# Kernel optimization log

Hardware: AMD Instinct MI355X
Metric: run time of the kernel (lower is better)

## Reference

```python
import jax, jax.numpy as jnp
import numpy as np

N = 10000      # atoms
E = 320000     # edges (avg degree 32)
C = 128        # hidden_channels
NB = 32        # num_basis
L = 3          # num_layers
CUT = 5.0      # cutoff
G = 8          # graphs in batch


def setup_inputs() -> dict:
    key = jax.random.key(0)
    ks = jax.random.split(key, 32)
    pos = jax.random.normal(ks[0], (N, 3), dtype=jnp.float32) * 2.0
    z = jax.random.randint(ks[1], (N,), 0, 100)
    row = jax.random.randint(ks[2], (E,), 0, N)
    # avoid self-loops so edge_length > 0
    col = (row + 1 + jax.random.randint(ks[3], (E,), 0, N - 1)) % N
    edge_index = jnp.stack([row, col])
    shifts = jnp.zeros((E, 3), dtype=jnp.float32)
    batch_index = jnp.sort(jax.random.randint(ks[4], (N,), 0, G))
    s = 0.05
    p = lambda k, shape: jax.random.normal(k, shape, dtype=jnp.float32) * s
    return {
        'z': z, 'pos': pos, 'edge_index': edge_index, 'shifts': shifts,
        'batch_index': batch_index,
        'emb': p(ks[5], (100, C)),
        # message blocks (stacked over layers)
        'm_w1': p(ks[6], (L, C, C)), 'm_b1': p(ks[7], (L, C)),
        'm_w2': p(ks[8], (L, C, 3 * C)), 'm_b2': p(ks[9], (L, 3 * C)),
        'f_w': p(ks[10], (L, NB, 3 * C)), 'f_b': p(ks[11], (L, 3 * C)),
        # update blocks
        'u_w': p(ks[12], (L, C, C)), 'v_w': p(ks[13], (L, C, C)),
        'up_w1': p(ks[14], (L, 2 * C, C)), 'up_b1': p(ks[15], (L, C)),
        'up_w2': p(ks[16], (L, C, 3 * C)), 'up_b2': p(ks[17], (L, 3 * C)),
        # readout
        'r_w1': p(ks[18], (C, C // 2)), 'r_b1': p(ks[19], (C // 2,)),
        'r_w2': p(ks[20], (C // 2, 1)), 'r_b2': p(ks[21], (1,)),
    }


def painn_energy(pos, shifts, emb, m_w1, m_b1, m_w2, m_b2, f_w, f_b,
                 u_w, v_w, up_w1, up_b1, up_w2, up_b2,
                 r_w1, r_b1, r_w2, r_b2, z, edge_index, batch_index):
    row, col = edge_index[0], edge_index[1]
    scalar = emb[z]                                  # [N, C]
    vector = jnp.zeros((N, 3, C), dtype=pos.dtype)   # [N, 3, C]

    edge_vec = pos[col] - pos[row] + shifts          # [E, 3]
    edge_len = jnp.sqrt(jnp.sum(edge_vec * edge_vec, axis=-1) + 1e-12)  # [E]
    direction = edge_vec / edge_len[:, None]

    # smooth bump envelope (C-inf, compact support)
    scaled = edge_len / CUT
    inside = scaled < 1.0
    denom = jnp.where(inside, 1.0 - scaled * scaled, 1.0)
    gate = jnp.where(inside, jnp.exp(1.0 - 1.0 / denom), 0.0)  # [E]

    # gaussian radial basis
    centers = jnp.linspace(0.0, CUT, NB)
    gamma = 1.0 / (centers[1] - centers[0]) ** 2
    rbf = jnp.exp(-gamma * (edge_len[:, None] - centers) ** 2)  # [E, NB]
    edge_attr = rbf * gate[:, None]

    for l in range(L):
        # --- message ---
        h = jax.nn.silu(scalar[col] @ m_w1[l] + m_b1[l]) @ m_w2[l] + m_b2[l]  # [E, 3C]
        w = h * (edge_attr @ f_w[l] + f_b[l]) * gate[:, None]
        w1, w2, w3 = jnp.split(w, 3, axis=-1)                                 # each [E, C]
        d_scalar = jax.ops.segment_sum(w1, row, num_segments=N)
        msg_vec = vector[col] * w2[:, None, :] + w3[:, None, :] * direction[:, :, None]  # [E,3,C]
        d_vector = jax.ops.segment_sum(msg_vec, row, num_segments=N)
        scalar = scalar + d_scalar
        vector = vector + d_vector
        # --- update ---
        uv = vector @ u_w[l]                                   # [N, 3, C]
        vv = vector @ v_w[l]
        v_norm = jnp.sqrt(jnp.sum(vv * vv, axis=1) + 1e-8)     # [N, C]
        a = jax.nn.silu(jnp.concatenate([scalar, v_norm], axis=-1) @ up_w1[l] + up_b1[l]) @ up_w2[l] + up_b2[l]
        a1, a2, a3 = jnp.split(a, 3, axis=-1)
        scalar = scalar + a1 + a2 * jnp.sum(uv * vv, axis=1)
        vector = vector + a3[:, None, :] * uv

    e_atom = jax.nn.silu(scalar @ r_w1 + r_b1) @ r_w2 + r_b2   # [N, 1]
    return jax.ops.segment_sum(e_atom, batch_index, num_segments=G)  # [G, 1]


def reference(z, pos, edge_index, shifts, batch_index, emb,
              m_w1, m_b1, m_w2, m_b2, f_w, f_b,
              u_w, v_w, up_w1, up_b1, up_w2, up_b2,
              r_w1, r_b1, r_w2, r_b2):
    return painn_energy(pos, shifts, emb, m_w1, m_b1, m_w2, m_b2, f_w, f_b,
                        u_w, v_w, up_w1, up_b1, up_w2, up_b2,
                        r_w1, r_b1, r_w2, r_b2, z, edge_index, batch_index)
```

## Files before the change

kernel.cpp:

```cpp
#include <hip/hip_runtime.h>
#include <math.h>

#define CUTR 5.0f
#define TL 2048
#define NBASIS 32
#define HSC 16.0f
#define TSC 16.0f
#define VSC 64.0f
#define INV_HT (1.0f / (HSC * TSC))
#define INV_HTV (1.0f / (HSC * TSC * VSC))

typedef __attribute__((ext_vector_type(8))) short bf16x8;
typedef __attribute__((ext_vector_type(4))) float f32x4;
typedef __attribute__((ext_vector_type(2))) float f32x2;

struct U3 { uint x, y, z; };

__device__ __forceinline__ float silu_f(float x) { return x / (1.0f + expf(-x)); }
__device__ __forceinline__ ushort f2bf(float x) {
  uint b = __float_as_uint(x);
  uint r = (b + 0x7FFFu + ((b >> 16) & 1u)) >> 16;
  return (ushort)r;
}
__device__ __forceinline__ float bf2f(ushort u) { return __uint_as_float((uint)u << 16); }
__device__ __forceinline__ uchar f2fp8(float x) {
  return (uchar)(__builtin_amdgcn_cvt_pk_fp8_f32(x, 0.0f, 0, false) & 0xff);
}
__device__ __forceinline__ f32x2 fp8lo(uint u) {
  return __builtin_amdgcn_cvt_pk_f32_fp8((int)u, false);
}
__device__ __forceinline__ f32x2 fp8hi(uint u) {
  return __builtin_amdgcn_cvt_pk_f32_fp8((int)u, true);
}

__global__ __launch_bounds__(384) void table_kernel(const float* __restrict__ f_w,
                                                    const float* __restrict__ f_b,
                                                    uchar* __restrict__ tab) {
  __shared__ float fws[NBASIS * 384];
  __shared__ float rbf[8][NBASIS];
  __shared__ float gv[8];
  int tid = threadIdx.x;
  int bi = blockIdx.x;
  int l = bi >> 8, tb = bi & 255;
  for (int i = tid; i < NBASIS * 384; i += 384) fws[i] = f_w[l * NBASIS * 384 + i];
  if (tid < 256) {
    int tt = tid >> 5, k = tid & 31;
    float len = (float)(tb * 8 + tt) * (CUTR / (float)(TL - 1));
    const float gamma = (31.0f / 5.0f) * (31.0f / 5.0f);
    float c = 5.0f * (float)k / 31.0f;
    float d = len - c;
    rbf[tt][k] = expf(-gamma * d * d);
    if (k == 0) {
      float s = len * (1.0f / CUTR);
      gv[tt] = (s < 1.0f) ? expf(1.0f - 1.0f / (1.0f - s * s)) : 0.0f;
    }
  }
  __syncthreads();
  int j = tid % 384;
  int b = j >> 7, ch = j & 127;
  float fb = f_b[l * 384 + j];
  for (int tt = 0; tt < 8; ++tt) {
    float acc = 0.0f;
#pragma unroll
    for (int k = 0; k < NBASIS; ++k) acc += rbf[tt][k] * fws[k * 384 + j];
    float g = gv[tt];
    tab[((size_t)l * TL + (size_t)(tb * 8 + tt)) * 512 + (ch >> 1) * 8 + b * 2 + (ch & 1)] =
        f2fp8(g * (g * acc + fb) * TSC);
  }
}

__global__ __launch_bounds__(256) void init_kernel(
    const int* __restrict__ z, const float* __restrict__ emb, float* __restrict__ scalar,
    ushort* __restrict__ sbf, const float* __restrict__ m_w1, const float* __restrict__ m_w2,
    const float* __restrict__ u_w, const float* __restrict__ v_w,
    const float* __restrict__ up_w1, const float* __restrict__ up_w2,
    const float* __restrict__ r_w1, ushort* __restrict__ wt, const float* __restrict__ pos,
    const int* __restrict__ ei, const float* __restrict__ shifts, int* __restrict__ counts,
    int N, int E) {
  int tid = threadIdx.x;
  int bi = blockIdx.x;
  int nbEmb = (N * 128 + 255) / 256;
  int nbW = (548864 + 255) / 256;
  if (bi < nbEmb) {
    int idx = bi * 256 + tid;
    if (idx >= N * 128) return;
    int n = idx >> 7, j = idx & 127;
    float v = emb[z[n] * 128 + j];
    scalar[idx] = v;
    sbf[idx] = f2bf(v);
    return;
  }
  bi -= nbEmb;
  if (bi < nbW) {
    int idx = bi * 256 + tid;
    if (idx >= 548864) return;
    float v;
    if (idx >= 540672) {
      int t = idx - 540672;
      int n = t >> 7, k = t & 127;
      v = r_w1[k * 64 + n];
    } else {
      int l = idx / 180224, local = idx % 180224;
      if (local < 16384) {
        int n = local >> 7, k = local & 127;
        v = m_w1[l * 16384 + k * 128 + n];
      } else if (local < 65536) {
        int t = local - 16384;
        int n = t >> 7, k = t & 127;
        v = m_w2[l * 49152 + k * 384 + n];
      } else if (local < 98304) {
        int t = local - 65536;
        int n = t >> 7, k = t & 127;
        v = (n < 128) ? u_w[l * 16384 + k * 128 + n] : v_w[l * 16384 + k * 128 + (n - 128)];
      } else if (local < 131072) {
        int t = local - 98304;
        int n = t >> 8, k = t & 255;
        v = up_w1[l * 32768 + k * 128 + n];
      } else {
        int t = local - 131072;
        int n = t >> 7, k = t & 127;
        v = up_w2[l * 49152 + k * 384 + n];
      }
    }
    wt[idx] = f2bf(v);
    return;
  }
  bi -= nbW;
  {
    int e = bi * 256 + tid;
    if (e >= E) return;
    int r = ei[e], c = ei[E + e];
    float dx = pos[c * 3 + 0] - pos[r * 3 + 0] + shifts[e * 3 + 0];
    float dy = pos[c * 3 + 1] - pos[r * 3 + 1] + shifts[e * 3 + 1];
    float dz = pos[c * 3 + 2] - pos[r * 3 + 2] + shifts[e * 3 + 2];
    float len = sqrtf(dx * dx + dy * dy + dz * dz + 1e-12f);
    if (len < CUTR) atomicAdd(&counts[r], 1);
  }
}

__global__ __launch_bounds__(1024) void scan_kernel(const int* __restrict__ counts,
                                                    int* __restrict__ offs,
                                                    int* __restrict__ cursor, int N) {
  __shared__ int sm[1024];
  int tid = threadIdx.x;
  int CH = (N + 1023) / 1024;
  int base = tid * CH;
  int sum = 0;
  for (int i = 0; i < CH; i++) sum += (base + i < N) ? counts[base + i] : 0;
  sm[tid] = sum;
  __syncthreads();
  for (int o = 1; o < 1024; o <<= 1) {
    int v = (tid >= o) ? sm[tid - o] : 0;
    __syncthreads();
    sm[tid] += v;
    __syncthreads();
  }
  int run = sm[tid] - sum;
  for (int i = 0; i < CH; i++) {
    if (base + i < N) {
      offs[base + i] = run;
      cursor[base + i] = run;
      run += counts[base + i];
    }
  }
  if (tid == 1023) offs[N] = sm[1023];
}

__global__ void fill_kernel(const float* __restrict__ pos, const int* __restrict__ ei,
                            const float* __restrict__ shifts, int* __restrict__ cursor,
                            float4* __restrict__ pk, int E) {
  int e = blockIdx.x * 256 + threadIdx.x;
  if (e >= E) return;
  int r = ei[e], c = ei[E + e];
  float dx = pos[c * 3 + 0] - pos[r * 3 + 0] + shifts[e * 3 + 0];
  float dy = pos[c * 3 + 1] - pos[r * 3 + 1] + shifts[e * 3 + 1];
  float dz = pos[c * 3 + 2] - pos[r * 3 + 2] + shifts[e * 3 + 2];
  float len = sqrtf(dx * dx + dy * dy + dz * dz + 1e-12f);
  if (len >= CUTR) return;
  float inv = 1.0f / len;
  float x = len * ((float)(TL - 1) / CUTR);
  int ib = (int)(x + 0.5f);
  if (ib > TL - 1) ib = TL - 1;
  int p = atomicAdd(&cursor[r], 1);
  pk[p] = make_float4(__int_as_float(c | (ib << 14)), dx * inv, dy * inv, dz * inv);
}

__global__ __launch_bounds__(256) void message_kernel(
    const int* __restrict__ offs, const float4* __restrict__ pk, const uchar* __restrict__ hv8,
    const uchar* __restrict__ tab8, float* __restrict__ scalar, ushort* __restrict__ sbf,
    float* __restrict__ vec, ushort* __restrict__ vbout, int N) {
  int lane = threadIdx.x & 63;
  int n = blockIdx.x * 4 + (threadIdx.x >> 6);
  if (n >= N) return;
  int p0 = offs[n], p1 = offs[n + 1];
  float aS0 = 0.f, aS1 = 0.f;
  float aW00 = 0.f, aW01 = 0.f, aW10 = 0.f, aW11 = 0.f, aW20 = 0.f, aW21 = 0.f;
  float aD00 = 0.f, aD01 = 0.f, aD10 = 0.f, aD11 = 0.f, aD20 = 0.f, aD21 = 0.f;
  int p = p0;
  bool hasA = p < p1, hasB = p + 1 < p1;
  float4 cA, cB;
  if (hasA) cA = pk[p];
  if (hasB) cB = pk[p + 1];
  while (hasA) {
    int bitsA = __float_as_int(cA.x);
    int colA = bitsA & 16383, ibA = bitsA >> 14;
    U3 hvA = *(const U3*)(hv8 + (size_t)colA * 768 + lane * 12);
    uint2 tA = *(const uint2*)(tab8 + (size_t)ibA * 512 + lane * 8);
    U3 hvB;
    uint2 tB;
    float4 dB;
    if (hasB) {
      int bitsB = __float_as_int(cB.x);
      int colB = bitsB & 16383, ibB = bitsB >> 14;
      dB = cB;
      hvB = *(const U3*)(hv8 + (size_t)colB * 768 + lane * 12);
      tB = *(const uint2*)(tab8 + (size_t)ibB * 512 + lane * 8);
    }
    int pn = p + 2;
    bool nA = pn < p1, nB = pn + 1 < p1;
    float4 fA, fB;
    if (nA) fA = pk[pn];
    if (nB) fB = pk[pn + 1];
    {
      f32x2 h1 = fp8lo(hvA.x), h2 = fp8hi(hvA.x);
      f32x2 h3 = fp8lo(hvA.y), v0 = fp8hi(hvA.y);
      f32x2 v1 = fp8lo(hvA.z), v2 = fp8hi(hvA.z);
      f32x2 t1 = fp8lo(tA.x), t2 = fp8hi(tA.x), t3 = fp8lo(tA.y);
      aS0 += h1.x * t1.x;
      aS1 += h1.y * t1.y;
      float w2l = h2.x * t2.x, w2h = h2.y * t2.y;
      float w3l = h3.x * t3.x, w3h = h3.y * t3.y;
      aW00 += v0.x * w2l; aW01 += v0.y * w2h;
      aW10 += v1.x * w2l; aW11 += v1.y * w2h;
      aW20 += v2.x * w2l; aW21 += v2.y * w2h;
      aD00 += w3l * cA.y; aD01 += w3h * cA.y;
      aD10 += w3l * cA.z; aD11 += w3h * cA.z;
      aD20 += w3l * cA.w; aD21 += w3h * cA.w;
    }
    if (hasB) {
      f32x2 h1 = fp8lo(hvB.x), h2 = fp8hi(hvB.x);
      f32x2 h3 = fp8lo(hvB.y), v0 = fp8hi(hvB.y);
      f32x2 v1 = fp8lo(hvB.z), v2 = fp8hi(hvB.z);
      f32x2 t1 = fp8lo(tB.x), t2 = fp8hi(tB.x), t3 = fp8lo(tB.y);
      aS0 += h1.x * t1.x;
      aS1 += h1.y * t1.y;
      float w2l = h2.x * t2.x, w2h = h2.y * t2.y;
      float w3l = h3.x * t3.x, w3h = h3.y * t3.y;
      aW00 += v0.x * w2l; aW01 += v0.y * w2h;
      aW10 += v1.x * w2l; aW11 += v1.y * w2h;
      aW20 += v2.x * w2l; aW21 += v2.y * w2h;
      aD00 += w3l * dB.y; aD01 += w3h * dB.y;
      aD10 += w3l * dB.z; aD11 += w3h * dB.z;
      aD20 += w3l * dB.w; aD21 += w3h * dB.w;
    }
    cA = fA;
    cB = fB;
    hasA = nA;
    hasB = nB;
    p = pn;
  }
  float sS0 = aS0 * INV_HT, sS1 = aS1 * INV_HT;
  float sV00 = aW00 * INV_HTV + aD00 * INV_HT;
  float sV01 = aW01 * INV_HTV + aD01 * INV_HT;
  float sV10 = aW10 * INV_HTV + aD10 * INV_HT;
  float sV11 = aW11 * INV_HTV + aD11 * INV_HT;
  float sV20 = aW20 * INV_HTV + aD20 * INV_HT;
  float sV21 = aW21 * INV_HTV + aD21 * INV_HT;
  float2* sp = (float2*)(scalar + (size_t)n * 128) + lane;
  float2 sv = *sp;
  sv.x += sS0;
  sv.y += sS1;
  *sp = sv;
  ((uint*)(sbf + (size_t)n * 128))[lane] = (uint)f2bf(sv.x) | ((uint)f2bf(sv.y) << 16);
  float2* vp0 = (float2*)(vec + (size_t)n * 384) + lane;
  float2* vp1 = (float2*)(vec + (size_t)n * 384 + 128) + lane;
  float2* vp2 = (float2*)(vec + (size_t)n * 384 + 256) + lane;
  float2 v0 = *vp0, v1 = *vp1, v2 = *vp2;
  v0.x += sV00; v0.y += sV01;
  v1.x += sV10; v1.y += sV11;
  v2.x += sV20; v2.y += sV21;
  *vp0 = v0; *vp1 = v1; *vp2 = v2;
  uint* ob = (uint*)(vbout + (size_t)n * 384);
  ob[lane] = (uint)f2bf(v0.x) | ((uint)f2bf(v0.y) << 16);
  ob[lane + 64] = (uint)f2bf(v1.x) | ((uint)f2bf(v1.y) << 16);
  ob[lane + 128] = (uint)f2bf(v2.x) | ((uint)f2bf(v2.y) << 16);
}

__global__ __launch_bounds__(512) void mlp_kernel(const ushort* __restrict__ A,
                                                  const ushort* __restrict__ W1T,
                                                  const float* __restrict__ b1,
                                                  const ushort* __restrict__ W2T,
                                                  const float* __restrict__ b2,
                                                  uchar* __restrict__ out, int M) {
  __shared__ ushort As[32 * 128];
  __shared__ ushort Bs[128 * 128];
  __shared__ ushort Hs[32 * 128];
  int tid = threadIdx.x;
  int lane = tid & 63, w = tid >> 6;
  int mh = w >> 2, wc = w & 3;
  int m0 = blockIdx.x * 32;
  int cl = lane & 15, rq = lane >> 4;
  int ra = mh * 16 + cl;
  f32x4 acc[2] = {};
  {
    {
      int row = tid >> 4, ch = tid & 15;
      uint4 av = make_uint4(0, 0, 0, 0);
      if (m0 + row < M) av = *(const uint4*)(A + (size_t)(m0 + row) * 128 + ch * 8);
      *(uint4*)(&As[row * 128 + ((ch ^ (row & 7)) * 8)]) = av;
    }
#pragma unroll
    for (int r = 0; r < 4; ++r) {
      int c = tid + r * 512;
      int row = c >> 4, ch = c & 15;
      uint4 bv = *(const uint4*)(W1T + (size_t)row * 128 + ch * 8);
      *(uint4*)(&Bs[row * 128 + ((ch ^ (row & 7)) * 8)]) = bv;
    }
    __syncthreads();
#pragma unroll
    for (int ks = 0; ks < 4; ++ks) {
      int ch = ks * 4 + rq;
      bf16x8 a = *(bf16x8*)&As[ra * 128 + ((ch ^ (ra & 7)) * 8)];
#pragma unroll
      for (int ns = 0; ns < 2; ++ns) {
        int rb = wc * 32 + ns * 16 + cl;
        bf16x8 b = *(bf16x8*)&Bs[rb * 128 + ((ch ^ (rb & 7)) * 8)];
        acc[ns] = __builtin_amdgcn_mfma_f32_16x16x32_bf16(a, b, acc[ns], 0, 0, 0);
      }
    }
  }
#pragma unroll
  for (int ns = 0; ns < 2; ++ns) {
    int hcol = wc * 32 + ns * 16 + cl;
    float bv = b1[hcol];
    int chunk = hcol >> 3, el = hcol & 7;
#pragma unroll
    for (int j = 0; j < 4; ++j) {
      int hr = mh * 16 + rq * 4 + j;
      float v = silu_f(acc[ns][j] + bv);
      Hs[hr * 128 + ((chunk ^ (hr & 7)) * 8) + el] = f2bf(v);
    }
  }
  __syncthreads();
  for (int nt = 0; nt < 3; ++nt) {
#pragma unroll
    for (int r = 0; r < 4; ++r) {
      int c = tid + r * 512;
      int row = c >> 4, ch = c & 15;
      uint4 bv = *(const uint4*)(W2T + (size_t)(nt * 128 + row) * 128 + ch * 8);
      *(uint4*)(&Bs[row * 128 + ((ch ^ (row & 7)) * 8)]) = bv;
    }
    __syncthreads();
    f32x4 acc2[2] = {};
#pragma unroll
    for (int ks = 0; ks < 4; ++ks) {
      int ch = ks * 4 + rq;
      bf16x8 a = *(bf16x8*)&Hs[ra * 128 + ((ch ^ (ra & 7)) * 8)];
#pragma unroll
      for (int ns = 0; ns < 2; ++ns) {
        int rb = wc * 32 + ns * 16 + cl;
        bf16x8 b = *(bf16x8*)&Bs[rb * 128 + ((ch ^ (rb & 7)) * 8)];
        acc2[ns] = __builtin_amdgcn_mfma_f32_16x16x32_bf16(a, b, acc2[ns], 0, 0, 0);
      }
    }
#pragma unroll
    for (int ns = 0; ns < 2; ++ns) {
      int ch = wc * 32 + ns * 16 + cl;
      float bv = b2[nt * 128 + ch];
#pragma unroll
      for (int j = 0; j < 4; ++j) {
        int m = m0 + mh * 16 + rq * 4 + j;
        if (m >= M) continue;
        out[(size_t)m * 768 + (ch >> 1) * 12 + nt * 2 + (ch & 1)] =
            f2fp8((acc2[ns][j] + bv) * HSC);
      }
    }
    __syncthreads();
  }
}

__global__ __launch_bounds__(512) void mlp2_kernel(const ushort* __restrict__ sbf_in,
                                                   const ushort* __restrict__ W1T,
                                                   const float* __restrict__ b1,
                                                   const ushort* __restrict__ W2T,
                                                   const float* __restrict__ b2,
                                                   const ushort* __restrict__ uvvv,
                                                   float* __restrict__ scalar,
                                                   ushort* __restrict__ sbf,
                                                   float* __restrict__ vec,
                                                   uchar* __restrict__ vbf8, int M) {
  __shared__ ushort As[32 * 128];
  __shared__ ushort Bs[128 * 128];
  __shared__ ushort Hs[32 * 128];
  int tid = threadIdx.x;
  int lane = tid & 63, w = tid >> 6;
  int mh = w >> 2, wc = w & 3;
  int m0 = blockIdx.x * 32;
  int cl = lane & 15, rq = lane >> 4;
  int ra = mh * 16 + cl;
  f32x4 acc[2] = {};
  for (int k0 = 0; k0 < 256; k0 += 128) {
    __syncthreads();
    {
      int row = tid >> 4, ch = tid & 15;
      uint4 av = make_uint4(0, 0, 0, 0);
      if (m0 + row < M) {
        if (k0 == 0) {
          av = *(const uint4*)(sbf_in + (size_t)(m0 + row) * 128 + ch * 8);
        } else {
          const ushort* ub = uvvv + (size_t)(m0 + row) * 768 + 128 + ch * 8;
          bf16x8 x0 = *(const bf16x8*)(ub);
          bf16x8 x1 = *(const bf16x8*)(ub + 256);
          bf16x8 x2 = *(const bf16x8*)(ub + 512);
          ushort pkv[8];
#pragma unroll
          for (int e = 0; e < 8; ++e) {
            float a = bf2f((ushort)x0[e]), bb = bf2f((ushort)x1[e]), cc = bf2f((ushort)x2[e]);
            pkv[e] = f2bf(sqrtf(a * a + bb * bb + cc * cc + 1e-8f));
          }
          av = *(uint4*)pkv;
        }
      }
      *(uint4*)(&As[row * 128 + ((ch ^ (row & 7)) * 8)]) = av;
    }
#pragma unroll
    for (int r = 0; r < 4; ++r) {
      int c = tid + r * 512;
      int row = c >> 4, ch = c & 15;
      uint4 bv = *(const uint4*)(W1T + (size_t)row * 256 + k0 + ch * 8);
      *(uint4*)(&Bs[row * 128 + ((ch ^ (row & 7)) * 8)]) = bv;
    }
    __syncthreads();
#pragma unroll
    for (int ks = 0; ks < 4; ++ks) {
      int ch = ks * 4 + rq;
      bf16x8 a = *(bf16x8*)&As[ra * 128 + ((ch ^ (ra & 7)) * 8)];
#pragma unroll
      for (int ns = 0; ns < 2; ++ns) {
        int rb = wc * 32 + ns * 16 + cl;
        bf16x8 b = *(bf16x8*)&Bs[rb * 128 + ((ch ^ (rb & 7)) * 8)];
        acc[ns] = __builtin_amdgcn_mfma_f32_16x16x32_bf16(a, b, acc[ns], 0, 0, 0);
      }
    }
  }
#pragma unroll
  for (int ns = 0; ns < 2; ++ns) {
    int hcol = wc * 32 + ns * 16 + cl;
    float bv = b1[hcol];
    int chunk = hcol >> 3, el = hcol & 7;
#pragma unroll
    for (int j = 0; j < 4; ++j) {
      int hr = mh * 16 + rq * 4 + j;
      float v = silu_f(acc[ns][j] + bv);
      Hs[hr * 128 + ((chunk ^ (hr & 7)) * 8) + el] = f2bf(v);
    }
  }
  __syncthreads();
  f32x4 aReg[3][2];
  for (int nt = 0; nt < 3; ++nt) {
#pragma unroll
    for (int r = 0; r < 4; ++r) {
      int c = tid + r * 512;
      int row = c >> 4, ch = c & 15;
      uint4 bv = *(const uint4*)(W2T + (size_t)(nt * 128 + row) * 128 + ch * 8);
      *(uint4*)(&Bs[row * 128 + ((ch ^ (row & 7)) * 8)]) = bv;
    }
    __syncthreads();
    f32x4 acc2[2] = {};
#pragma unroll
    for (int ks = 0; ks < 4; ++ks) {
      int ch = ks * 4 + rq;
      bf16x8 a = *(bf16x8*)&Hs[ra * 128 + ((ch ^ (ra & 7)) * 8)];
#pragma unroll
      for (int ns = 0; ns < 2; ++ns) {
        int rb = wc * 32 + ns * 16 + cl;
        bf16x8 b = *(bf16x8*)&Bs[rb * 128 + ((ch ^ (rb & 7)) * 8)];
        acc2[ns] = __builtin_amdgcn_mfma_f32_16x16x32_bf16(a, b, acc2[ns], 0, 0, 0);
      }
    }
#pragma unroll
    for (int ns = 0; ns < 2; ++ns) aReg[nt][ns] = acc2[ns];
    __syncthreads();
  }
#pragma unroll
  for (int ns = 0; ns < 2; ++ns) {
    int chOff = wc * 32 + ns * 16 + cl;
    float b2a = b2[chOff], b2b = b2[128 + chOff], b2c = b2[256 + chOff];
#pragma unroll
    for (int j = 0; j < 4; ++j) {
      int nn = m0 + mh * 16 + rq * 4 + j;
      if (nn >= M) continue;
      float a1 = aReg[0][ns][j] + b2a;
      float a2 = aReg[1][ns][j] + b2b;
      float a3 = aReg[2][ns][j] + b2c;
      const ushort* ub = uvvv + (size_t)nn * 768;
      float uv0 = bf2f(ub[chOff]), vv0 = bf2f(ub[128 + chOff]);
      float uv1 = bf2f(ub[256 + chOff]), vv1 = bf2f(ub[384 + chOff]);
      float uv2 = bf2f(ub[512 + chOff]), vv2 = bf2f(ub[640 + chOff]);
      float dot = uv0 * vv0 + uv1 * vv1 + uv2 * vv2;
      size_t si = (size_t)nn * 128 + chOff;
      float s = scalar[si] + a1 + a2 * dot;
      scalar[si] = s;
      sbf[si] = f2bf(s);
      size_t vb = (size_t)nn * 384 + chOff;
      float nv0 = vec[vb] + a3 * uv0;
      float nv1 = vec[vb + 128] + a3 * uv1;
      float nv2 = vec[vb + 256] + a3 * uv2;
      vec[vb] = nv0;
      vec[vb + 128] = nv1;
      vec[vb + 256] = nv2;
      size_t hb = (size_t)nn * 768 + (chOff >> 1) * 12 + 6 + (chOff & 1);
      vbf8[hb] = f2fp8(nv0 * VSC);
      vbf8[hb + 2] = f2fp8(nv1 * VSC);
      vbf8[hb + 4] = f2fp8(nv2 * VSC);
    }
  }
}

__global__ __launch_bounds__(256) void gemm_kernel(const ushort* __restrict__ A,
                                                   const ushort* __restrict__ WT,
                                                   ushort* __restrict__ Cout, int M, int K,
                                                   int Nn) {
  __shared__ ushort As[64 * 128];
  __shared__ ushort Bs[64 * 128];
  int tid = threadIdx.x;
  int m0 = blockIdx.x * 64, n0 = blockIdx.y * 64;
  int lane = tid & 63, w = tid >> 6, wr = w >> 1, wc = w & 1;
  f32x4 acc[2][2] = {};
  for (int k0 = 0; k0 < K; k0 += 128) {
    __syncthreads();
#pragma unroll
    for (int r = 0; r < 4; ++r) {
      int c = tid + r * 256;
      int row = c >> 4, col16 = c & 15;
      uint4 av = make_uint4(0, 0, 0, 0);
      if (m0 + row < M) av = *(const uint4*)(A + (size_t)(m0 + row) * K + k0 + col16 * 8);
      *(uint4*)(&As[row * 128 + ((col16 ^ (row & 7)) * 8)]) = av;
      uint4 bv = *(const uint4*)(WT + (size_t)(n0 + row) * K + k0 + col16 * 8);
      *(uint4*)(&Bs[row * 128 + ((col16 ^ (row & 7)) * 8)]) = bv;
    }
    __syncthreads();
#pragma unroll
    for (int ks = 0; ks < 4; ++ks) {
      int ch = ks * 4 + (lane >> 4);
      int ra0 = wr * 32 + (lane & 15), ra1 = ra0 + 16;
      int rb0 = wc * 32 + (lane & 15), rb1 = rb0 + 16;
      bf16x8 a0 = *(bf16x8*)&As[ra0 * 128 + ((ch ^ (ra0 & 7)) * 8)];
      bf16x8 a1 = *(bf16x8*)&As[ra1 * 128 + ((ch ^ (ra1 & 7)) * 8)];
      bf16x8 b0 = *(bf16x8*)&Bs[rb0 * 128 + ((ch ^ (rb0 & 7)) * 8)];
      bf16x8 b1 = *(bf16x8*)&Bs[rb1 * 128 + ((ch ^ (rb1 & 7)) * 8)];
      acc[0][0] = __builtin_amdgcn_mfma_f32_16x16x32_bf16(a0, b0, acc[0][0], 0, 0, 0);
      acc[0][1] = __builtin_amdgcn_mfma_f32_16x16x32_bf16(a0, b1, acc[0][1], 0, 0, 0);
      acc[1][0] = __builtin_amdgcn_mfma_f32_16x16x32_bf16(a1, b0, acc[1][0], 0, 0, 0);
      acc[1][1] = __builtin_amdgcn_mfma_f32_16x16x32_bf16(a1, b1, acc[1][1], 0, 0, 0);
    }
  }
  int cl = lane & 15, rq = lane >> 4;
#pragma unroll
  for (int ms = 0; ms < 2; ++ms)
#pragma unroll
    for (int ns = 0; ns < 2; ++ns) {
      int n = n0 + wc * 32 + ns * 16 + cl;
#pragma unroll
      for (int j = 0; j < 4; ++j) {
        int m = m0 + wr * 32 + ms * 16 + rq * 4 + j;
        if (m >= M) continue;
        Cout[(size_t)m * Nn + n] = f2bf(acc[ms][ns][j]);
      }
    }
}

__global__ __launch_bounds__(256) void readout_kernel(
    const ushort* __restrict__ sbf, const ushort* __restrict__ r1T, const float* __restrict__ rb1,
    const float* __restrict__ r_w2, const float* __restrict__ r_b2, const int* __restrict__ bidx,
    float* __restrict__ out, int N, int G) {
  __shared__ ushort As[64 * 128];
  __shared__ ushort Bs[64 * 128];
  __shared__ float rs[64];
  __shared__ float sm[64];
  int tid = threadIdx.x;
  int m0 = blockIdx.x * 64;
  int lane = tid & 63, w = tid >> 6, wr = w >> 1, wc = w & 1;
  int cl = lane & 15, rq = lane >> 4;
#pragma unroll
  for (int r = 0; r < 4; ++r) {
    int c = tid + r * 256;
    int row = c >> 4, ch = c & 15;
    uint4 av = make_uint4(0, 0, 0, 0);
    if (m0 + row < N) av = *(const uint4*)(sbf + (size_t)(m0 + row) * 128 + ch * 8);
    *(uint4*)(&As[row * 128 + ((ch ^ (row & 7)) * 8)]) = av;
    uint4 bv = *(const uint4*)(r1T + (size_t)row * 128 + ch * 8);
    *(uint4*)(&Bs[row * 128 + ((ch ^ (row & 7)) * 8)]) = bv;
  }
  if (tid < 64) {
    rs[tid] = 0.f;
    sm[tid] = 0.f;
  }
  __syncthreads();
  f32x4 acc[2][2] = {};
#pragma unroll
  for (int ks = 0; ks < 4; ++ks) {
    int ch = ks * 4 + rq;
    int ra0 = wr * 32 + cl, ra1 = ra0 + 16;
    int rb0 = wc * 32 + cl, rb1 = rb0 + 16;
    bf16x8 a0 = *(bf16x8*)&As[ra0 * 128 + ((ch ^ (ra0 & 7)) * 8)];
    bf16x8 a1 = *(bf16x8*)&As[ra1 * 128 + ((ch ^ (ra1 & 7)) * 8)];
    bf16x8 b0 = *(bf16x8*)&Bs[rb0 * 128 + ((ch ^ (rb0 & 7)) * 8)];
    bf16x8 b1 = *(bf16x8*)&Bs[rb1 * 128 + ((ch ^ (rb1 & 7)) * 8)];
    acc[0][0] = __builtin_amdgcn_mfma_f32_16x16x32_bf16(a0, b0, acc[0][0], 0, 0, 0);
    acc[0][1] = __builtin_amdgcn_mfma_f32_16x16x32_bf16(a0, b1, acc[0][1], 0, 0, 0);
    acc[1][0] = __builtin_amdgcn_mfma_f32_16x16x32_bf16(a1, b0, acc[1][0], 0, 0, 0);
    acc[1][1] = __builtin_amdgcn_mfma_f32_16x16x32_bf16(a1, b1, acc[1][1], 0, 0, 0);
  }
#pragma unroll
  for (int ms = 0; ms < 2; ++ms) {
    float part0 = 0.f, part1 = 0.f, part2 = 0.f, part3 = 0.f;
#pragma unroll
    for (int ns = 0; ns < 2; ++ns) {
      int col = wc * 32 + ns * 16 + cl;
      float b1v = rb1[col], wv = r_w2[col];
      part0 += silu_f(acc[ms][ns][0] + b1v) * wv;
      part1 += silu_f(acc[ms][ns][1] + b1v) * wv;
      part2 += silu_f(acc[ms][ns][2] + b1v) * wv;
      part3 += silu_f(acc[ms][ns][3] + b1v) * wv;
    }
#pragma unroll
    for (int o = 1; o < 16; o <<= 1) {
      part0 += __shfl_xor(part0, o);
      part1 += __shfl_xor(part1, o);
      part2 += __shfl_xor(part2, o);
      part3 += __shfl_xor(part3, o);
    }
    if (cl == 0) {
      int rbase = wr * 32 + ms * 16 + rq * 4;
      atomicAdd(&rs[rbase + 0], part0);
      atomicAdd(&rs[rbase + 1], part1);
      atomicAdd(&rs[rbase + 2], part2);
      atomicAdd(&rs[rbase + 3], part3);
    }
  }
  __syncthreads();
  float rb2 = r_b2[0];
  if (tid < 64) {
    int m = m0 + tid;
    if (m < N) atomicAdd(&sm[bidx[m]], rs[tid] + rb2);
  }
  __syncthreads();
  if (tid < G && G <= 64) atomicAdd(&out[tid], sm[tid]);
}

extern "C" void kernel_launch(void* const* d_in, const int* in_sizes, int n_in, void* d_out,
                              int out_size, void* d_ws, size_t ws_size, hipStream_t stream) {
  const int N = in_sizes[0];
  const int E = in_sizes[2] / 2;
  const int G = out_size;

  const int* z = (const int*)d_in[0];
  const float* pos = (const float*)d_in[1];
  const int* ei = (const int*)d_in[2];
  const float* shifts = (const float*)d_in[3];
  const int* bidx = (const int*)d_in[4];
  const float* emb = (const float*)d_in[5];
  const float* m_w1 = (const float*)d_in[6];
  const float* m_b1 = (const float*)d_in[7];
  const float* m_w2 = (const float*)d_in[8];
  const float* m_b2 = (const float*)d_in[9];
  const float* f_w = (const float*)d_in[10];
  const float* f_b = (const float*)d_in[11];
  const float* u_w = (const float*)d_in[12];
  const float* v_w = (const float*)d_in[13];
  const float* up_w1 = (const float*)d_in[14];
  const float* up_b1 = (const float*)d_in[15];
  const float* up_w2 = (const float*)d_in[16];
  const float* up_b2 = (const float*)d_in[17];
  const float* r_w1 = (const float*)d_in[18];
  const float* r_b1 = (const float*)d_in[19];
  const float* r_w2 = (const float*)d_in[20];
  const float* r_b2 = (const float*)d_in[21];
  float* out = (float*)d_out;

  float* w = (float*)d_ws;
  size_t off = 0;
  auto alloc = [&](size_t nfl) { float* p = w + off; off += (nfl + 3) & ~(size_t)3; return p; };
  uchar* tab8 = (uchar*)alloc((size_t)3 * TL * 128);
  float* scalar = alloc((size_t)N * 128);
  ushort* sbf = (ushort*)alloc((size_t)N * 64);
  float* vec = alloc((size_t)N * 384);
  uchar* hv8 = (uchar*)alloc((size_t)N * 192);
  ushort* mir_bf = (ushort*)alloc((size_t)N * 192);
  ushort* uvvv = (ushort*)alloc((size_t)N * 384);
  float* pkf = alloc((size_t)E * 4);
  ushort* wt = (ushort*)alloc((size_t)274432);
  int* counts = (int*)alloc((size_t)N);
  int* offs = (int*)alloc((size_t)N + 4);
  int* cursor = (int*)alloc((size_t)N);
  if (off * sizeof(float) > ws_size) return;

  hipMemsetAsync(counts, 0, (size_t)N * sizeof(int), stream);
  hipMemsetAsync(vec, 0, (size_t)N * 384 * sizeof(float), stream);
  hipMemsetAsync(hv8, 0, (size_t)N * 768, stream);
  hipMemsetAsync(out, 0, (size_t)G * sizeof(float), stream);

  table_kernel<<<3 * (TL / 8), 384, 0, stream>>>(f_w, f_b, tab8);
  int nbEmb = (N * 128 + 255) / 256;
  int nbW = (548864 + 255) / 256;
  int nbCount = (E + 255) / 256;
  init_kernel<<<nbEmb + nbW + nbCount, 256, 0, stream>>>(z, emb, scalar, sbf, m_w1, m_w2, u_w,
                                                         v_w, up_w1, up_w2, r_w1, wt, pos, ei,
                                                         shifts, counts, N, E);
  scan_kernel<<<1, 1024, 0, stream>>>(counts, offs, cursor, N);
  fill_kernel<<<(E + 255) / 256, 256, 0, stream>>>(pos, ei, shifts, cursor, (float4*)pkf, E);

  dim3 gm((N + 31) / 32);
  dim3 g3((3 * N + 63) / 64, 4);

  for (int l = 0; l < 3; l++) {
    const ushort* wl = wt + (size_t)l * 180224;
    mlp_kernel<<<gm, 512, 0, stream>>>(sbf, wl, m_b1 + l * 128, wl + 16384, m_b2 + l * 384,
                                       hv8, N);
    message_kernel<<<(N + 3) / 4, 256, 0, stream>>>(
        offs, (const float4*)pkf, hv8, tab8 + (size_t)l * TL * 512, scalar, sbf, vec, mir_bf, N);
    gemm_kernel<<<g3, 256, 0, stream>>>(mir_bf, wl + 65536, uvvv, 3 * N, 128, 256);
    mlp2_kernel<<<gm, 512, 0, stream>>>(sbf, wl + 98304, up_b1 + l * 128, wl + 131072,
                                        up_b2 + l * 384, uvvv, scalar, sbf, vec, hv8, N);
  }

  readout_kernel<<<(N + 63) / 64, 256, 0, stream>>>(sbf, wt + 540672, r_b1, r_w2, r_b2, bidx,
                                                    out, N, G);
}
```

Baseline: 340.9 us.

## Fuse next-layer message MLP into update kernel and specialize first/last layers

The next layer's message MLP (scalar -> hidden -> 3C filter) now runs inside mlp2_kernel, reusing the freshly updated bf16 scalars staged in shared memory, so a separate mlp_kernel launch and its reload of sbf are dropped for layers 1 and 2. The first message_kernel is templated to skip loading and using the vector part of hv8, and to write vec directly instead of read-modify-write, since the vector is zero at that point. This allows removing the memsets of vec and hv8. The last update skips the vector and hv8 writes. The cost is higher register and shared-memory pressure in the fused kernel.

```diff
diff --git a/kernel.cpp b/kernel.cpp
--- a/kernel.cpp
+++ b/kernel.cpp
@@ -15,6 +15,7 @@
 typedef __attribute__((ext_vector_type(2))) float f32x2;
 
 struct U3 { uint x, y, z; };
+struct U2 { uint x, y; };
 
 __device__ __forceinline__ float silu_f(float x) { return x / (1.0f + expf(-x)); }
 __device__ __forceinline__ ushort f2bf(float x) {
@@ -185,6 +186,7 @@
   pk[p] = make_float4(__int_as_float(c | (ib << 14)), dx * inv, dy * inv, dz * inv);
 }
 
+template <bool FIRST>
 __global__ __launch_bounds__(256) void message_kernel(
     const int* __restrict__ offs, const float4* __restrict__ pk, const uchar* __restrict__ hv8,
     const uchar* __restrict__ tab8, float* __restrict__ scalar, ushort* __restrict__ sbf,
@@ -204,17 +206,28 @@
   while (hasA) {
     int bitsA = __float_as_int(cA.x);
     int colA = bitsA & 16383, ibA = bitsA >> 14;
-    U3 hvA = *(const U3*)(hv8 + (size_t)colA * 768 + lane * 12);
-    uint2 tA = *(const uint2*)(tab8 + (size_t)ibA * 512 + lane * 8);
+    U3 hvA;
+    if (FIRST) {
+      U2 t = *(const U2*)(hv8 + (size_t)colA * 768 + lane * 12);
+      hvA.x = t.x; hvA.y = t.y; hvA.z = 0;
+    } else {
+      hvA = *(const U3*)(hv8 + (size_t)colA * 768 + lane * 12);
+    }
+    U2 tA = *(const U2*)(tab8 + (size_t)ibA * 512 + lane * 8);
     U3 hvB;
-    uint2 tB;
+    U2 tB;
     float4 dB;
     if (hasB) {
       int bitsB = __float_as_int(cB.x);
       int colB = bitsB & 16383, ibB = bitsB >> 14;
       dB = cB;
-      hvB = *(const U3*)(hv8 + (size_t)colB * 768 + lane * 12);
-      tB = *(const uint2*)(tab8 + (size_t)ibB * 512 + lane * 8);
+      if (FIRST) {
+        U2 t = *(const U2*)(hv8 + (size_t)colB * 768 + lane * 12);
+        hvB.x = t.x; hvB.y = t.y; hvB.z = 0;
+      } else {
+        hvB = *(const U3*)(hv8 + (size_t)colB * 768 + lane * 12);
+      }
+      tB = *(const U2*)(tab8 + (size_t)ibB * 512 + lane * 8);
     }
     int pn = p + 2;
     bool nA = pn < p1, nB = pn + 1 < p1;
@@ -223,32 +236,36 @@
     if (nB) fB = pk[pn + 1];
     {
       f32x2 h1 = fp8lo(hvA.x), h2 = fp8hi(hvA.x);
-      f32x2 h3 = fp8lo(hvA.y), v0 = fp8hi(hvA.y);
-      f32x2 v1 = fp8lo(hvA.z), v2 = fp8hi(hvA.z);
+      f32x2 h3 = fp8lo(hvA.y);
       f32x2 t1 = fp8lo(tA.x), t2 = fp8hi(tA.x), t3 = fp8lo(tA.y);
       aS0 += h1.x * t1.x;
       aS1 += h1.y * t1.y;
-      float w2l = h2.x * t2.x, w2h = h2.y * t2.y;
       float w3l = h3.x * t3.x, w3h = h3.y * t3.y;
-      aW00 += v0.x * w2l; aW01 += v0.y * w2h;
-      aW10 += v1.x * w2l; aW11 += v1.y * w2h;
-      aW20 += v2.x * w2l; aW21 += v2.y * w2h;
+      if (!FIRST) {
+        f32x2 v0 = fp8hi(hvA.y), v1 = fp8lo(hvA.z), v2 = fp8hi(hvA.z);
+        float w2l = h2.x * t2.x, w2h = h2.y * t2.y;
+        aW00 += v0.x * w2l; aW01 += v0.y * w2h;
+        aW10 += v1.x * w2l; aW11 += v1.y * w2h;
+        aW20 += v2.x * w2l; aW21 += v2.y * w2h;
+      }
       aD00 += w3l * cA.y; aD01 += w3h * cA.y;
       aD10 += w3l * cA.z; aD11 += w3h * cA.z;
       aD20 += w3l * cA.w; aD21 += w3h * cA.w;
     }
     if (hasB) {
       f32x2 h1 = fp8lo(hvB.x), h2 = fp8hi(hvB.x);
-      f32x2 h3 = fp8lo(hvB.y), v0 = fp8hi(hvB.y);
-      f32x2 v1 = fp8lo(hvB.z), v2 = fp8hi(hvB.z);
+      f32x2 h3 = fp8lo(hvB.y);
       f32x2 t1 = fp8lo(tB.x), t2 = fp8hi(tB.x), t3 = fp8lo(tB.y);
       aS0 += h1.x * t1.x;
       aS1 += h1.y * t1.y;
-      float w2l = h2.x * t2.x, w2h = h2.y * t2.y;
       float w3l = h3.x * t3.x, w3h = h3.y * t3.y;
-      aW00 += v0.x * w2l; aW01 += v0.y * w2h;
-      aW10 += v1.x * w2l; aW11 += v1.y * w2h;
-      aW20 += v2.x * w2l; aW21 += v2.y * w2h;
+      if (!FIRST) {
+        f32x2 v0 = fp8hi(hvB.y), v1 = fp8lo(hvB.z), v2 = fp8hi(hvB.z);
+        float w2l = h2.x * t2.x, w2h = h2.y * t2.y;
+        aW00 += v0.x * w2l; aW01 += v0.y * w2h;
+        aW10 += v1.x * w2l; aW11 += v1.y * w2h;
+        aW20 += v2.x * w2l; aW21 += v2.y * w2h;
+      }
       aD00 += w3l * dB.y; aD01 += w3h * dB.y;
       aD10 += w3l * dB.z; aD11 += w3h * dB.z;
       aD20 += w3l * dB.w; aD21 += w3h * dB.w;
@@ -260,12 +277,14 @@
     p = pn;
   }
   float sS0 = aS0 * INV_HT, sS1 = aS1 * INV_HT;
-  float sV00 = aW00 * INV_HTV + aD00 * INV_HT;
-  float sV01 = aW01 * INV_HTV + aD01 * INV_HT;
-  float sV10 = aW10 * INV_HTV + aD10 * INV_HT;
-  float sV11 = aW11 * INV_HTV + aD11 * INV_HT;
-  float sV20 = aW20 * INV_HTV + aD20 * INV_HT;
-  float sV21 = aW21 * INV_HTV + aD21 * INV_HT;
+  float sV00 = aD00 * INV_HT, sV01 = aD01 * INV_HT;
+  float sV10 = aD10 * INV_HT, sV11 = aD11 * INV_HT;
+  float sV20 = aD20 * INV_HT, sV21 = aD21 * INV_HT;
+  if (!FIRST) {
+    sV00 += aW00 * INV_HTV; sV01 += aW01 * INV_HTV;
+    sV10 += aW10 * INV_HTV; sV11 += aW11 * INV_HTV;
+    sV20 += aW20 * INV_HTV; sV21 += aW21 * INV_HTV;
+  }
   float2* sp = (float2*)(scalar + (size_t)n * 128) + lane;
   float2 sv = *sp;
   sv.x += sS0;
@@ -275,10 +294,17 @@
   float2* vp0 = (float2*)(vec + (size_t)n * 384) + lane;
   float2* vp1 = (float2*)(vec + (size_t)n * 384 + 128) + lane;
   float2* vp2 = (float2*)(vec + (size_t)n * 384 + 256) + lane;
-  float2 v0 = *vp0, v1 = *vp1, v2 = *vp2;
-  v0.x += sV00; v0.y += sV01;
-  v1.x += sV10; v1.y += sV11;
-  v2.x += sV20; v2.y += sV21;
+  float2 v0, v1, v2;
+  if (FIRST) {
+    v0 = make_float2(sV00, sV01);
+    v1 = make_float2(sV10, sV11);
+    v2 = make_float2(sV20, sV21);
+  } else {
+    v0 = *vp0; v1 = *vp1; v2 = *vp2;
+    v0.x += sV00; v0.y += sV01;
+    v1.x += sV10; v1.y += sV11;
+    v2.x += sV20; v2.y += sV21;
+  }
   *vp0 = v0; *vp1 = v1; *vp2 = v2;
   uint* ob = (uint*)(vbout + (size_t)n * 384);
   ob[lane] = (uint)f2bf(v0.x) | ((uint)f2bf(v0.y) << 16);
@@ -379,16 +405,14 @@
   }
 }
 
-__global__ __launch_bounds__(512) void mlp2_kernel(const ushort* __restrict__ sbf_in,
-                                                   const ushort* __restrict__ W1T,
-                                                   const float* __restrict__ b1,
-                                                   const ushort* __restrict__ W2T,
-                                                   const float* __restrict__ b2,
-                                                   const ushort* __restrict__ uvvv,
-                                                   float* __restrict__ scalar,
-                                                   ushort* __restrict__ sbf,
-                                                   float* __restrict__ vec,
-                                                   uchar* __restrict__ vbf8, int M) {
+template <bool LAST>
+__global__ __launch_bounds__(512) void mlp2_kernel(
+    const ushort* __restrict__ sbf_in, const ushort* __restrict__ W1T,
+    const float* __restrict__ b1, const ushort* __restrict__ W2T, const float* __restrict__ b2,
+    const ushort* __restrict__ uvvv, float* __restrict__ scalar, ushort* __restrict__ sbf,
+    float* __restrict__ vec, uchar* __restrict__ hv8, const ushort* __restrict__ W1nT,
+    const float* __restrict__ b1n, const ushort* __restrict__ W2nT,
+    const float* __restrict__ b2n, int M) {
   __shared__ ushort As[32 * 128];
   __shared__ ushort Bs[128 * 128];
   __shared__ ushort Hs[32 * 128];
@@ -501,19 +525,93 @@
       size_t si = (size_t)nn * 128 + chOff;
       float s = scalar[si] + a1 + a2 * dot;
       scalar[si] = s;
-      sbf[si] = f2bf(s);
-      size_t vb = (size_t)nn * 384 + chOff;
-      float nv0 = vec[vb] + a3 * uv0;
-      float nv1 = vec[vb + 128] + a3 * uv1;
-      float nv2 = vec[vb + 256] + a3 * uv2;
-      vec[vb] = nv0;
-      vec[vb + 128] = nv1;
-      vec[vb + 256] = nv2;
-      size_t hb = (size_t)nn * 768 + (chOff >> 1) * 12 + 6 + (chOff & 1);
-      vbf8[hb] = f2fp8(nv0 * VSC);
-      vbf8[hb + 2] = f2fp8(nv1 * VSC);
-      vbf8[hb + 4] = f2fp8(nv2 * VSC);
-    }
+      ushort sb = f2bf(s);
+      sbf[si] = sb;
+      if (!LAST) {
+        int lr = mh * 16 + rq * 4 + j;
+        As[lr * 128 + (((chOff >> 3) ^ (lr & 7)) * 8) + (chOff & 7)] = sb;
+        size_t vb = (size_t)nn * 384 + chOff;
+        float nv0 = vec[vb] + a3 * uv0;
+        float nv1 = vec[vb + 128] + a3 * uv1;
+        float nv2 = vec[vb + 256] + a3 * uv2;
+        vec[vb] = nv0;
+        vec[vb + 128] = nv1;
+        vec[vb + 256] = nv2;
+        size_t hb = (size_t)nn * 768 + (chOff >> 1) * 12 + 6 + (chOff & 1);
+        hv8[hb] = f2fp8(nv0 * VSC);
+        hv8[hb + 2] = f2fp8(nv1 * VSC);
+        hv8[hb + 4] = f2fp8(nv2 * VSC);
+      }
+    }
+  }
+  if (LAST) return;
+#pragma unroll
+  for (int r = 0; r < 4; ++r) {
+    int c = tid + r * 512;
+    int row = c >> 4, ch = c & 15;
+    uint4 bv = *(const uint4*)(W1nT + (size_t)row * 128 + ch * 8);
+    *(uint4*)(&Bs[row * 128 + ((ch ^ (row & 7)) * 8)]) = bv;
+  }
+  __syncthreads();
+  f32x4 acc3[2] = {};
+#pragma unroll
+  for (int ks = 0; ks < 4; ++ks) {
+    int ch = ks * 4 + rq;
+    bf16x8 a = *(bf16x8*)&As[ra * 128 + ((ch ^ (ra & 7)) * 8)];
+#pragma unroll
+    for (int ns = 0; ns < 2; ++ns) {
+      int rb = wc * 32 + ns * 16 + cl;
+      bf16x8 b = *(bf16x8*)&Bs[rb * 128 + ((ch ^ (rb & 7)) * 8)];
+      acc3[ns] = __builtin_amdgcn_mfma_f32_16x16x32_bf16(a, b, acc3[ns], 0, 0, 0);
+    }
+  }
+  __syncthreads();
+#pragma unroll
+  for (int ns = 0; ns < 2; ++ns) {
+    int hcol = wc * 32 + ns * 16 + cl;
+    float bv = b1n[hcol];
+    int chunk = hcol >> 3, el = hcol & 7;
+#pragma unroll
+    for (int j = 0; j < 4; ++j) {
+      int hr = mh * 16 + rq * 4 + j;
+      Hs[hr * 128 + ((chunk ^ (hr & 7)) * 8) + el] = f2bf(silu_f(acc3[ns][j] + bv));
+    }
+  }
+  __syncthreads();
+  for (int nt = 0; nt < 3; ++nt) {
+#pragma unroll
+    for (int r = 0; r < 4; ++r) {
+      int c = tid + r * 512;
+      int row = c >> 4, ch = c & 15;
+      uint4 bv = *(const uint4*)(W2nT + (size_t)(nt * 128 + row) * 128 + ch * 8);
+      *(uint4*)(&Bs[row * 128 + ((ch ^ (row & 7)) * 8)]) = bv;
+    }
+    __syncthreads();
+    f32x4 acc4[2] = {};
+#pragma unroll
+    for (int ks = 0; ks < 4; ++ks) {
+      int ch = ks * 4 + rq;
+      bf16x8 a = *(bf16x8*)&Hs[ra * 128 + ((ch ^ (ra & 7)) * 8)];
+#pragma unroll
+      for (int ns = 0; ns < 2; ++ns) {
+        int rb = wc * 32 + ns * 16 + cl;
+        bf16x8 b = *(bf16x8*)&Bs[rb * 128 + ((ch ^ (rb & 7)) * 8)];
+        acc4[ns] = __builtin_amdgcn_mfma_f32_16x16x32_bf16(a, b, acc4[ns], 0, 0, 0);
+      }
+    }
+#pragma unroll
+    for (int ns = 0; ns < 2; ++ns) {
+      int ch = wc * 32 + ns * 16 + cl;
+      float bv = b2n[nt * 128 + ch];
+#pragma unroll
+      for (int j = 0; j < 4; ++j) {
+        int m = m0 + mh * 16 + rq * 4 + j;
+        if (m >= M) continue;
+        hv8[(size_t)m * 768 + (ch >> 1) * 12 + nt * 2 + (ch & 1)] =
+            f2fp8((acc4[ns][j] + bv) * HSC);
+      }
+    }
+    __syncthreads();
   }
 }
 
@@ -697,8 +795,6 @@
   if (off * sizeof(float) > ws_size) return;
 
   hipMemsetAsync(counts, 0, (size_t)N * sizeof(int), stream);
-  hipMemsetAsync(vec, 0, (size_t)N * 384 * sizeof(float), stream);
-  hipMemsetAsync(hv8, 0, (size_t)N * 768, stream);
   hipMemsetAsync(out, 0, (size_t)G * sizeof(float), stream);
 
   table_kernel<<<3 * (TL / 8), 384, 0, stream>>>(f_w, f_b, tab8);
@@ -714,15 +810,29 @@
   dim3 gm((N + 31) / 32);
   dim3 g3((3 * N + 63) / 64, 4);
 
+  mlp_kernel<<<gm, 512, 0, stream>>>(sbf, wt, m_b1, wt + 16384, m_b2, hv8, N);
+
   for (int l = 0; l < 3; l++) {
     const ushort* wl = wt + (size_t)l * 180224;
-    mlp_kernel<<<gm, 512, 0, stream>>>(sbf, wl, m_b1 + l * 128, wl + 16384, m_b2 + l * 384,
-                                       hv8, N);
-    message_kernel<<<(N + 3) / 4, 256, 0, stream>>>(
-        offs, (const float4*)pkf, hv8, tab8 + (size_t)l * TL * 512, scalar, sbf, vec, mir_bf, N);
+    if (l == 0)
+      message_kernel<true><<<(N + 3) / 4, 256, 0, stream>>>(
+          offs, (const float4*)pkf, hv8, tab8 + (size_t)l * TL * 512, scalar, sbf, vec, mir_bf,
+          N);
+    else
+      message_kernel<false><<<(N + 3) / 4, 256, 0, stream>>>(
+          offs, (const float4*)pkf, hv8, tab8 + (size_t)l * TL * 512, scalar, sbf, vec, mir_bf,
+          N);
     gemm_kernel<<<g3, 256, 0, stream>>>(mir_bf, wl + 65536, uvvv, 3 * N, 128, 256);
-    mlp2_kernel<<<gm, 512, 0, stream>>>(sbf, wl + 98304, up_b1 + l * 128, wl + 131072,
-                                        up_b2 + l * 384, uvvv, scalar, sbf, vec, hv8, N);
+    if (l < 2) {
+      const ushort* wn = wt + (size_t)(l + 1) * 180224;
+      mlp2_kernel<false><<<gm, 512, 0, stream>>>(
+          sbf, wl + 98304, up_b1 + l * 128, wl + 131072, up_b2 + l * 384, uvvv, scalar, sbf, vec,
+          hv8, wn, m_b1 + (l + 1) * 128, wn + 16384, m_b2 + (l + 1) * 384, N);
+    } else {
+      mlp2_kernel<true><<<gm, 512, 0, stream>>>(
+          sbf, wl + 98304, up_b1 + l * 128, wl + 131072, up_b2 + l * 384, uvvv, scalar, sbf, vec,
+          hv8, wt, m_b1, wt, m_b2, N);
+    }
   }
 
   readout_kernel<<<(N + 63) / 64, 256, 0, stream>>>(sbf, wt + 540672, r_b1, r_w2, r_b2, bidx,
```

Result: faster. 312.8 us (-8.2%).
